# Kernel optimization log

Hardware: AMD Instinct MI355X
Metric: run time of the kernel (lower is better)

## Reference

```python
import jax, jax.numpy as jnp
import numpy as np

N = 100000   # nodes
E = 1600000  # edges
F = 13       # input features
H = 128      # hidden dim
G = 512      # graphs in batch
C = 10       # classes
EPS = 1e-5   # BatchNorm eps


def setup_inputs() -> dict:
    key = jax.random.key(0)
    ks = jax.random.split(key, 12)
    inp = {
        "x": jax.random.normal(ks[0], (N, F), dtype=jnp.float32),
        "edge_index": jax.random.randint(ks[1], (2, E), 0, N, dtype=jnp.int64),
        "batch": jnp.sort(jax.random.randint(ks[2], (N,), 0, G, dtype=jnp.int64)),
        "W1": jax.random.normal(ks[3], (F, H), dtype=jnp.float32) / np.sqrt(F),
        "b1": jnp.zeros((H,), jnp.float32),
        "g1": jnp.ones((H,), jnp.float32), "be1": jnp.zeros((H,), jnp.float32),
        "m1": jnp.zeros((H,), jnp.float32), "v1": jnp.ones((H,), jnp.float32),
        "W2": jax.random.normal(ks[4], (H, H), dtype=jnp.float32) / np.sqrt(H),
        "b2": jnp.zeros((H,), jnp.float32),
        "g2": jnp.ones((H,), jnp.float32), "be2": jnp.zeros((H,), jnp.float32),
        "m2": jnp.zeros((H,), jnp.float32), "v2": jnp.ones((H,), jnp.float32),
        "W3": jax.random.normal(ks[5], (H, H), dtype=jnp.float32) / np.sqrt(H),
        "b3": jnp.zeros((H,), jnp.float32),
        "g3": jnp.ones((H,), jnp.float32), "be3": jnp.zeros((H,), jnp.float32),
        "m3": jnp.zeros((H,), jnp.float32), "v3": jnp.ones((H,), jnp.float32),
        "Wc1": jax.random.normal(ks[6], (H, H // 2), dtype=jnp.float32) / np.sqrt(H),
        "bc1": jnp.zeros((H // 2,), jnp.float32),
        "Wc2": jax.random.normal(ks[7], (H // 2, C), dtype=jnp.float32) / np.sqrt(H // 2),
        "bc2": jnp.zeros((C,), jnp.float32),
    }
    return inp


def reference(x, edge_index, batch,
              W1, b1, g1, be1, m1, v1,
              W2, b2, g2, be2, m2, v2,
              W3, b3, g3, be3, m3, v3,
              Wc1, bc1, Wc2, bc2):
    src, dst = edge_index[0], edge_index[1]
    n = x.shape[0]
    # GCN symmetric norm with self-loops: deg = in-degree(A) + 1
    deg = jax.ops.segment_sum(jnp.ones(src.shape[0], x.dtype), dst, num_segments=n) + 1.0
    dis = jax.lax.rsqrt(deg)                    # D^{-1/2}
    enorm = dis[src] * dis[dst]                 # per-edge norm [E]
    snorm = dis * dis                           # self-loop norm [N]

    def gcn(h, W, b):
        h = h @ W                               # [N,H]
        msg = h[src] * enorm[:, None]           # gather + scale [E,H]
        agg = jax.ops.segment_sum(msg, dst, num_segments=n)  # scatter-add
        return agg + h * snorm[:, None] + b

    def bn(h, g, be, m, v):                     # eval-mode BatchNorm1d
        return (h - m) * jax.lax.rsqrt(v + EPS) * g + be

    h = jax.nn.relu(bn(gcn(x, W1, b1), g1, be1, m1, v1))
    h = jax.nn.relu(bn(gcn(h, W2, b2), g2, be2, m2, v2))
    h = jax.nn.relu(bn(gcn(h, W3, b3), g3, be3, m3, v3))
    # dropout is identity in eval mode

    # global mean pool over graphs
    sums = jax.ops.segment_sum(h, batch, num_segments=G)            # [G,H]
    cnts = jax.ops.segment_sum(jnp.ones(n, h.dtype), batch, num_segments=G)
    pooled = sums / jnp.maximum(cnts, 1.0)[:, None]

    hid = jax.nn.relu(pooled @ Wc1 + bc1)
    logits = hid @ Wc2 + bc2                                        # [G,C]
    return logits
```

## Files before the change

### kernel.cpp

```cpp
#include <hip/hip_runtime.h>
#include <hip/hip_bf16.h>

#define EPS 1e-5f

typedef unsigned short u16;
typedef unsigned int u32;
typedef __attribute__((ext_vector_type(8))) short bf16x8;
typedef __attribute__((ext_vector_type(4))) float f32x4;

__device__ __forceinline__ u32 f2bf(float f) {
  u32 u = __float_as_uint(f);
  return (u + 0x7FFFu + ((u >> 16) & 1u)) >> 16;
}
__device__ __forceinline__ u32 pack2bf(float lo, float hi) {
  return f2bf(lo) | (f2bf(hi) << 16);
}

__device__ __forceinline__ void dacc(float2& a, u32 u) {
  a.x += __uint_as_float(u << 16);
  a.y += __uint_as_float(u & 0xFFFF0000u);
}

__global__ void k_hist_rank(const int* __restrict__ dst, int* __restrict__ cnt,
                            int* __restrict__ rank, int E) {
  int i = blockIdx.x * blockDim.x + threadIdx.x;
  int i4 = i << 2;
  if (i4 + 3 < E) {
    int d0 = dst[i4], d1 = dst[i4 + 1], d2 = dst[i4 + 2], d3 = dst[i4 + 3];
    int r0 = atomicAdd(&cnt[d0], 1);
    int r1 = atomicAdd(&cnt[d1], 1);
    int r2 = atomicAdd(&cnt[d2], 1);
    int r3 = atomicAdd(&cnt[d3], 1);
    rank[i4] = r0; rank[i4 + 1] = r1; rank[i4 + 2] = r2; rank[i4 + 3] = r3;
  } else {
    for (int e = i4; e < E; ++e) rank[e] = atomicAdd(&cnt[dst[e]], 1);
  }
}

__global__ void k_dis_pdeg(const int* __restrict__ cnt, float* __restrict__ dis,
                           int* __restrict__ pdeg, int N) {
  int i = blockIdx.x * blockDim.x + threadIdx.x;
  if (i < N) {
    int d = cnt[i];
    dis[i] = rsqrtf((float)d + 1.0f);
    pdeg[i] = (d + 3) & ~3;
  }
}

__global__ void k_scan_block(const int* __restrict__ in, int* __restrict__ out,
                             int* __restrict__ bsum, int N) {
  __shared__ int tmp[256];
  int lid = threadIdx.x;
  int i = blockIdx.x * 256 + lid;
  int v = (i < N) ? in[i] : 0;
  tmp[lid] = v;
  __syncthreads();
  for (int off = 1; off < 256; off <<= 1) {
    int t = (lid >= off) ? tmp[lid - off] : 0;
    __syncthreads();
    tmp[lid] += t;
    __syncthreads();
  }
  if (i < N) out[i] = tmp[lid] - v;
  if (lid == 255) bsum[blockIdx.x] = tmp[255];
}

__global__ void k_scan_bsum(const int* __restrict__ bsum, int* __restrict__ bexc, int nb) {
  __shared__ int tmp[512];
  int lid = threadIdx.x;
  int v = (lid < nb) ? bsum[lid] : 0;
  tmp[lid] = v;
  __syncthreads();
  for (int off = 1; off < 512; off <<= 1) {
    int t = (lid >= off) ? tmp[lid - off] : 0;
    __syncthreads();
    tmp[lid] += t;
    __syncthreads();
  }
  if (lid < nb) bexc[lid] = tmp[lid] - v;
}

__global__ void k_add_back(int* __restrict__ offs, const int* __restrict__ bexc,
                           const int* __restrict__ bsum, int N, int nb) {
  int i = blockIdx.x * 256 + threadIdx.x;
  if (i < N) offs[i] += bexc[blockIdx.x];
  if (i == 0) offs[N] = bexc[nb - 1] + bsum[nb - 1];
}

__global__ void k_fill_rank(const int* __restrict__ src, const int* __restrict__ dst,
                            const int* __restrict__ rank, const int* __restrict__ offs,
                            int* __restrict__ csr, int E) {
  int i = blockIdx.x * blockDim.x + threadIdx.x;
  int i4 = i << 2;
  if (i4 + 3 < E) {
    int s0 = src[i4], s1 = src[i4 + 1], s2 = src[i4 + 2], s3 = src[i4 + 3];
    int d0 = dst[i4], d1 = dst[i4 + 1], d2 = dst[i4 + 2], d3 = dst[i4 + 3];
    int r0 = rank[i4], r1 = rank[i4 + 1], r2 = rank[i4 + 2], r3 = rank[i4 + 3];
    csr[offs[d0] + r0] = s0;
    csr[offs[d1] + r1] = s1;
    csr[offs[d2] + r2] = s2;
    csr[offs[d3] + r3] = s3;
  } else {
    for (int e = i4; e < E; ++e) csr[offs[dst[e]] + rank[e]] = src[e];
  }
}

__global__ void k_pad_fill(const int* __restrict__ deg, const int* __restrict__ offs,
                           int* __restrict__ csr, int N) {
  int n = blockIdx.x * blockDim.x + threadIdx.x;
  if (n >= N) return;
  int b = offs[n] + deg[n], e = offs[n + 1];
  for (int j = b; j < e; ++j) csr[j] = N;
}

__global__ void k_prep_w(const float* __restrict__ W2, const float* __restrict__ W3,
                         const float* __restrict__ b2, const float* __restrict__ g2,
                         const float* __restrict__ be2, const float* __restrict__ m2,
                         const float* __restrict__ v2,
                         const float* __restrict__ b3, const float* __restrict__ g3,
                         const float* __restrict__ be3, const float* __restrict__ m3,
                         const float* __restrict__ v3,
                         u16* __restrict__ Wht2, u16* __restrict__ Wlt2,
                         u16* __restrict__ Wht3, u16* __restrict__ Wlt3,
                         float* __restrict__ sc2, float* __restrict__ tc2,
                         float* __restrict__ sc3, float* __restrict__ tc3) {
  int idx = blockIdx.x * 256 + threadIdx.x;
  int layer = idx >> 14;
  int e = idx & 16383;
  int c = e >> 7, k = e & 127;
  const float* W = layer ? W3 : W2;
  float w = W[k * 128 + c];
  u32 h = f2bf(w);
  float l = w - __uint_as_float(h << 16);
  u16* Wh = layer ? Wht3 : Wht2;
  u16* Wl = layer ? Wlt3 : Wlt2;
  Wh[e] = (u16)h;
  Wl[e] = (u16)f2bf(l);
  if (e < 128) {
    int ch = e;
    const float* gg = layer ? g3 : g2;  const float* vv = layer ? v3 : v2;
    const float* be = layer ? be3 : be2; const float* mm = layer ? m3 : m2;
    const float* bb = layer ? b3 : b2;
    float s = gg[ch] * rsqrtf(vv[ch] + EPS);
    (layer ? sc3 : sc2)[ch] = s;
    (layer ? tc3 : tc2)[ch] = be[ch] + (bb[ch] - mm[ch]) * s;
  }
}

__global__ void k_padx_scale(const float* __restrict__ x, const float* __restrict__ dis,
                             float* __restrict__ xs, int N) {
  int i = blockIdx.x * blockDim.x + threadIdx.x;
  if (i >= (N + 1) * 16) return;
  int n = i >> 4, f = i & 15;
  xs[i] = (n < N && f < 13) ? x[n * 13 + f] * dis[n] : 0.0f;
}

__global__ __launch_bounds__(64) void k_agg16(
    const float* __restrict__ xs, const int* __restrict__ csr,
    const int* __restrict__ offs, const float* __restrict__ dis,
    float* __restrict__ out, int N) {
  int node = (blockIdx.x << 2) + (threadIdx.x >> 4);
  if (node >= N) return;
  int f = threadIdx.x & 15;
  float a0 = xs[(size_t)node * 16 + f];
  float a1 = 0.f, a2 = 0.f, a3 = 0.f;
  int beg = offs[node], end = offs[node + 1];
  for (int i = beg; i < end; i += 4) {
    int4 s4 = *(const int4*)(csr + i);
    a0 += xs[(size_t)s4.x * 16 + f];
    a1 += xs[(size_t)s4.y * 16 + f];
    a2 += xs[(size_t)s4.z * 16 + f];
    a3 += xs[(size_t)s4.w * 16 + f];
  }
  out[(size_t)node * 16 + f] = dis[node] * ((a0 + a1) + (a2 + a3));
}

__global__ __launch_bounds__(256) void k_gemm1(
    const float* __restrict__ ax, const float* __restrict__ W1,
    const float* __restrict__ bb, const float* __restrict__ gg,
    const float* __restrict__ be, const float* __restrict__ mm,
    const float* __restrict__ vv, const float* __restrict__ dis,
    u32* __restrict__ outb, int N) {
  const int lane = threadIdx.x & 63;
  const int wid = blockIdx.x * (blockDim.x >> 6) + (threadIdx.x >> 6);
  const int nw = gridDim.x * (blockDim.x >> 6);
  const int c0 = lane * 2, c1 = c0 + 1;
  float s0 = gg[c0] * rsqrtf(vv[c0] + EPS);
  float t0 = be[c0] + (bb[c0] - mm[c0]) * s0;
  float s1 = gg[c1] * rsqrtf(vv[c1] + EPS);
  float t1 = be[c1] + (bb[c1] - mm[c1]) * s1;
  float w0[13], w1[13];
#pragma unroll
  for (int k = 0; k < 13; ++k) {
    w0[k] = W1[k * 128 + c0];
    w1[k] = W1[k * 128 + c1];
  }
  for (int node = wid; node <= N; node += nw) {
    if (node == N) { outb[(size_t)node * 64 + lane] = 0u; continue; }
    float4 A0 = *(const float4*)(ax + (size_t)node * 16);
    float4 A1 = *(const float4*)(ax + (size_t)node * 16 + 4);
    float4 A2 = *(const float4*)(ax + (size_t)node * 16 + 8);
    float  a12 = ax[(size_t)node * 16 + 12];
    float av[13] = {A0.x, A0.y, A0.z, A0.w, A1.x, A1.y, A1.z, A1.w,
                    A2.x, A2.y, A2.z, A2.w, a12};
    float acc0 = 0.f, acc1 = 0.f;
#pragma unroll
    for (int k = 0; k < 13; ++k) {
      acc0 = fmaf(av[k], w0[k], acc0);
      acc1 = fmaf(av[k], w1[k], acc1);
    }
    float dn = dis[node];
    float o0 = dn * fmaxf(fmaf(acc0, s0, t0), 0.f);
    float o1 = dn * fmaxf(fmaf(acc1, s1, t1), 0.f);
    outb[(size_t)node * 64 + lane] = pack2bf(o0, o1);
  }
}

__global__ __launch_bounds__(256) void k_agg128(
    const u16* __restrict__ hb, const int* __restrict__ csr,
    const int* __restrict__ offs, const float* __restrict__ dis,
    uint4* __restrict__ Ahp, uint4* __restrict__ Alp, int N) {
  int node = (blockIdx.x << 2) + (threadIdx.x >> 6);
  if (node >= N) return;
  node = __builtin_amdgcn_readfirstlane(node);
  const int lane = threadIdx.x & 63;
  const int qt = lane >> 4;
  const int q = lane & 15;
  const uint4* __restrict__ H = (const uint4*)hb;
  int beg = offs[node], end = offs[node + 1];

  float2 z2 = make_float2(0.f, 0.f);
  float2 aA0 = z2, aA1 = z2, aA2 = z2, aA3 = z2;
  float2 aB0 = z2, aB1 = z2, aB2 = z2, aB3 = z2;

  {
    uint4 su = H[(size_t)node * 16 + q];
    if (qt == 0) { dacc(aA0, su.x); dacc(aA1, su.y); dacc(aA2, su.z); dacc(aA3, su.w); }
  }

  int i = beg;
  for (; i + 8 <= end; i += 8) {
    int4 sA = *(const int4*)(csr + i);
    int4 sB = *(const int4*)(csr + i + 4);
    int ea = (qt == 0) ? sA.x : (qt == 1) ? sA.y : (qt == 2) ? sA.z : sA.w;
    int eb = (qt == 0) ? sB.x : (qt == 1) ? sB.y : (qt == 2) ? sB.z : sB.w;
    uint4 uA = H[(size_t)ea * 16 + q];
    uint4 uB = H[(size_t)eb * 16 + q];
    dacc(aA0, uA.x); dacc(aA1, uA.y); dacc(aA2, uA.z); dacc(aA3, uA.w);
    dacc(aB0, uB.x); dacc(aB1, uB.y); dacc(aB2, uB.z); dacc(aB3, uB.w);
  }
  if (i < end) {
    int4 sA = *(const int4*)(csr + i);
    int ea = (qt == 0) ? sA.x : (qt == 1) ? sA.y : (qt == 2) ? sA.z : sA.w;
    uint4 uA = H[(size_t)ea * 16 + q];
    dacc(aA0, uA.x); dacc(aA1, uA.y); dacc(aA2, uA.z); dacc(aA3, uA.w);
  }

  float r[8];
  r[0] = aA0.x + aB0.x; r[1] = aA0.y + aB0.y;
  r[2] = aA1.x + aB1.x; r[3] = aA1.y + aB1.y;
  r[4] = aA2.x + aB2.x; r[5] = aA2.y + aB2.y;
  r[6] = aA3.x + aB3.x; r[7] = aA3.y + aB3.y;
#pragma unroll
  for (int j = 0; j < 8; ++j) {
    r[j] += __shfl_xor(r[j], 16, 64);
    r[j] += __shfl_xor(r[j], 32, 64);
  }
  if (qt == 0) {
    float dn = dis[node];
    uint4 ph, pl;
    u32 hw[8];
#pragma unroll
    for (int j = 0; j < 8; ++j) { r[j] *= dn; hw[j] = f2bf(r[j]); }
    ph.x = hw[0] | (hw[1] << 16);
    ph.y = hw[2] | (hw[3] << 16);
    ph.z = hw[4] | (hw[5] << 16);
    ph.w = hw[6] | (hw[7] << 16);
    float l[8];
#pragma unroll
    for (int j = 0; j < 8; ++j) l[j] = r[j] - __uint_as_float(hw[j] << 16);
    pl.x = pack2bf(l[0], l[1]);
    pl.y = pack2bf(l[2], l[3]);
    pl.z = pack2bf(l[4], l[5]);
    pl.w = pack2bf(l[6], l[7]);
    Ahp[(size_t)node * 16 + q] = ph;
    Alp[(size_t)node * 16 + q] = pl;
  }
}

template <bool OB>
__global__ __launch_bounds__(256) void k_gemm_mfma(
    const u16* __restrict__ Ah, const u16* __restrict__ Al,
    const u16* __restrict__ Wht, const u16* __restrict__ Wlt,
    const float* __restrict__ sc, const float* __restrict__ tc,
    const float* __restrict__ dis,
    float* __restrict__ outf, u16* __restrict__ outb, int N) {
  const int lane = threadIdx.x & 63;
  const int wv = threadIdx.x >> 6;
  const int r0 = blockIdx.x * 128 + wv * 32;
  const int lr = lane & 15;
  const int kg = lane >> 4;

  bf16x8 ahf[2][4], alf[2][4];
#pragma unroll
  for (int rt = 0; rt < 2; ++rt) {
    int row = min(r0 + rt * 16 + lr, N - 1);
    const bf16x8* pAh = (const bf16x8*)(Ah + (size_t)row * 128 + kg * 8);
    const bf16x8* pAl = (const bf16x8*)(Al + (size_t)row * 128 + kg * 8);
#pragma unroll
    for (int ks = 0; ks < 4; ++ks) {
      ahf[rt][ks] = pAh[ks * 4];
      alf[rt][ks] = pAl[ks * 4];
    }
  }
  float dr[2][4];
  if (OB) {
#pragma unroll
    for (int rt = 0; rt < 2; ++rt)
#pragma unroll
      for (int j = 0; j < 4; ++j)
        dr[rt][j] = dis[min(r0 + rt * 16 + kg * 4 + j, N - 1)];
  }

#pragma unroll
  for (int ct = 0; ct < 8; ++ct) {
    int c = ct * 16 + lr;
    const bf16x8* pBh = (const bf16x8*)(Wht + (size_t)c * 128 + kg * 8);
    const bf16x8* pBl = (const bf16x8*)(Wlt + (size_t)c * 128 + kg * 8);
    bf16x8 bh[4], bl[4];
#pragma unroll
    for (int ks = 0; ks < 4; ++ks) { bh[ks] = pBh[ks * 4]; bl[ks] = pBl[ks * 4]; }
    float s = sc[c], t = tc[c];
#pragma unroll
    for (int rt = 0; rt < 2; ++rt) {
      f32x4 acc = {0.f, 0.f, 0.f, 0.f};
#pragma unroll
      for (int ks = 0; ks < 4; ++ks) {
        acc = __builtin_amdgcn_mfma_f32_16x16x32_bf16(ahf[rt][ks], bh[ks], acc, 0, 0, 0);
        acc = __builtin_amdgcn_mfma_f32_16x16x32_bf16(alf[rt][ks], bh[ks], acc, 0, 0, 0);
        acc = __builtin_amdgcn_mfma_f32_16x16x32_bf16(ahf[rt][ks], bl[ks], acc, 0, 0, 0);
      }
#pragma unroll
      for (int j = 0; j < 4; ++j) {
        int row = r0 + rt * 16 + kg * 4 + j;
        if (row < N) {
          float o = fmaxf(fmaf(acc[j], s, t), 0.f);
          if (OB) {
            outb[(size_t)row * 128 + c] = (u16)f2bf(o * dr[rt][j]);
          } else {
            outf[(size_t)row * 128 + c] = o;
          }
        }
      }
    }
  }
}

__global__ void k_cnt_batch(const int* __restrict__ batch, int* __restrict__ cnt,
                            int N, int G) {
  int g = blockIdx.x * blockDim.x + threadIdx.x;
  if (g >= G) return;
  int lo = 0, hi = N;
  while (lo < hi) { int m = (lo + hi) >> 1; if (batch[m] < g) lo = m + 1; else hi = m; }
  int lb = lo;
  lo = 0; hi = N;
  while (lo < hi) { int m = (lo + hi) >> 1; if (batch[m] <= g) lo = m + 1; else hi = m; }
  cnt[g] = lo - lb;
}

__global__ __launch_bounds__(128) void k_pool(
    const float* __restrict__ h, const int* __restrict__ batch,
    float* __restrict__ pooled, int N) {
  int f = threadIdx.x;
  int n0 = blockIdx.x * 128;
  int nEnd = min(n0 + 128, N);
  float acc = 0.f;
  int cur = -1;
  for (int nn = n0; nn < nEnd; ++nn) {
    int g = batch[nn];
    if (g != cur) {
      if (cur >= 0) atomicAdd(&pooled[cur * 128 + f], acc);
      cur = g;
      acc = 0.f;
    }
    acc += h[(size_t)nn * 128 + f];
  }
  if (cur >= 0) atomicAdd(&pooled[cur * 128 + f], acc);
}

__global__ __launch_bounds__(64) void k_cls(
    const float* __restrict__ pooled, const int* __restrict__ cnt,
    const float* __restrict__ Wc1, const float* __restrict__ bc1,
    const float* __restrict__ Wc2, const float* __restrict__ bc2,
    float* __restrict__ out, int G) {
  __shared__ float pm[128];
  __shared__ float hid[64];
  int g = blockIdx.x, t = threadIdx.x;
  float invc = 1.f / fmaxf((float)cnt[g], 1.f);
  pm[t]      = pooled[g * 128 + t] * invc;
  pm[t + 64] = pooled[g * 128 + 64 + t] * invc;
  __syncthreads();
  float a = bc1[t];
#pragma unroll 8
  for (int k = 0; k < 128; ++k) a = fmaf(pm[k], Wc1[k * 64 + t], a);
  hid[t] = fmaxf(a, 0.f);
  __syncthreads();
  if (t < 10) {
    float a2 = bc2[t];
#pragma unroll
    for (int j = 0; j < 64; ++j) a2 = fmaf(hid[j], Wc2[j * 10 + t], a2);
    out[g * 10 + t] = a2;
  }
}

extern "C" void kernel_launch(void* const* d_in, const int* in_sizes, int n_in,
                              void* d_out, int out_size, void* d_ws, size_t ws_size,
                              hipStream_t stream) {
  const float* x   = (const float*)d_in[0];
  const int*   ei  = (const int*)d_in[1];
  const int* batch = (const int*)d_in[2];
  const float* W1 = (const float*)d_in[3];
  const float* b1 = (const float*)d_in[4];
  const float* g1 = (const float*)d_in[5];
  const float* be1 = (const float*)d_in[6];
  const float* m1 = (const float*)d_in[7];
  const float* v1 = (const float*)d_in[8];
  const float* W2 = (const float*)d_in[9];
  const float* b2 = (const float*)d_in[10];
  const float* g2 = (const float*)d_in[11];
  const float* be2 = (const float*)d_in[12];
  const float* m2 = (const float*)d_in[13];
  const float* v2 = (const float*)d_in[14];
  const float* W3 = (const float*)d_in[15];
  const float* b3 = (const float*)d_in[16];
  const float* g3 = (const float*)d_in[17];
  const float* be3 = (const float*)d_in[18];
  const float* m3 = (const float*)d_in[19];
  const float* v3 = (const float*)d_in[20];
  const float* Wc1 = (const float*)d_in[21];
  const float* bc1 = (const float*)d_in[22];
  const float* Wc2 = (const float*)d_in[23];
  const float* bc2 = (const float*)d_in[24];

  const int N = in_sizes[0] / 13;
  const int E = in_sizes[1] / 2;
  const int G = out_size / 10;
  const int* src = ei;
  const int* dst = ei + E;

  char* ws = (char*)d_ws;
  size_t off = 0;
  auto alloc = [&](size_t bytes) {
    char* p = ws + off;
    off = (off + bytes + 255) & ~(size_t)255;
    return p;
  };
  int*   deg    = (int*)  alloc((size_t)N * 4);
  float* dis    = (float*)alloc((size_t)N * 4);
  int*   pdeg   = (int*)  alloc((size_t)N * 4);
  int*   offs   = (int*)  alloc((size_t)(N + 1) * 4);
  const int nb  = (N + 255) / 256;
  int*   bsum   = (int*)  alloc((size_t)nb * 4);
  int*   bexc   = (int*)  alloc((size_t)nb * 4);
  int*   rank   = (int*)  alloc((size_t)E * 4);
  int*   csr    = (int*)  alloc(((size_t)E + 3 * (size_t)N + 8) * 4);
  u16*   hbf    = (u16*)  alloc((size_t)(N + 1) * 128 * 2);
  u16*   Ahp    = (u16*)  alloc((size_t)N * 128 * 2);
  u16*   Alp    = (u16*)  alloc((size_t)N * 128 * 2);
  float* bufF   = (float*)alloc((size_t)(N + 1) * 128 * 4);
  u16*   Wht2   = (u16*)  alloc(16384 * 2);
  u16*   Wlt2   = (u16*)  alloc(16384 * 2);
  u16*   Wht3   = (u16*)  alloc(16384 * 2);
  u16*   Wlt3   = (u16*)  alloc(16384 * 2);
  float* sc2    = (float*)alloc(128 * 4);
  float* tc2    = (float*)alloc(128 * 4);
  float* sc3    = (float*)alloc(128 * 4);
  float* tc3    = (float*)alloc(128 * 4);
  float* pooled = (float*)alloc((size_t)G * 128 * 4);
  int*   cntg   = (int*)  alloc((size_t)G * 4);
  float* xs = bufF;
  float* ax = (float*)Ahp;

  hipMemsetAsync(deg, 0, (size_t)N * 4, stream);
  hipMemsetAsync(pooled, 0, (size_t)G * 128 * 4, stream);

  k_prep_w<<<128, 256, 0, stream>>>(W2, W3, b2, g2, be2, m2, v2, b3, g3, be3, m3, v3,
                                    Wht2, Wlt2, Wht3, Wlt3, sc2, tc2, sc3, tc3);

  const int nE4 = (E + 3) / 4;
  k_hist_rank<<<(nE4 + 255) / 256, 256, 0, stream>>>(dst, deg, rank, E);
  k_dis_pdeg<<<(N + 255) / 256, 256, 0, stream>>>(deg, dis, pdeg, N);
  k_scan_block<<<nb, 256, 0, stream>>>(pdeg, offs, bsum, N);
  k_scan_bsum<<<1, 512, 0, stream>>>(bsum, bexc, nb);
  k_add_back<<<nb, 256, 0, stream>>>(offs, bexc, bsum, N, nb);
  k_fill_rank<<<(nE4 + 255) / 256, 256, 0, stream>>>(src, dst, rank, offs, csr, E);
  k_pad_fill<<<(N + 255) / 256, 256, 0, stream>>>(deg, offs, csr, N);

  k_padx_scale<<<((N + 1) * 16 + 255) / 256, 256, 0, stream>>>(x, dis, xs, N);
  k_agg16<<<(N + 3) / 4, 64, 0, stream>>>(xs, csr, offs, dis, ax, N);
  k_gemm1<<<1024, 256, 0, stream>>>(ax, W1, b1, g1, be1, m1, v1, dis, (u32*)hbf, N);

  const int gemmGrid = (N + 127) / 128;
  k_agg128<<<(N + 3) / 4, 256, 0, stream>>>(hbf, csr, offs, dis,
                                            (uint4*)Ahp, (uint4*)Alp, N);
  k_gemm_mfma<true><<<gemmGrid, 256, 0, stream>>>(Ahp, Alp, Wht2, Wlt2, sc2, tc2, dis,
                                                  nullptr, hbf, N);
  k_agg128<<<(N + 3) / 4, 256, 0, stream>>>(hbf, csr, offs, dis,
                                            (uint4*)Ahp, (uint4*)Alp, N);
  k_gemm_mfma<false><<<gemmGrid, 256, 0, stream>>>(Ahp, Alp, Wht3, Wlt3, sc3, tc3, dis,
                                                   bufF, nullptr, N);

  k_cnt_batch<<<(G + 255) / 256, 256, 0, stream>>>(batch, cntg, N, G);
  k_pool<<<(N + 127) / 128, 128, 0, stream>>>(bufF, batch, pooled, N);
  k_cls<<<G, 64, 0, stream>>>(pooled, cntg, Wc1, bc1, Wc2, bc2, (float*)d_out, G);
}
```

Measured before the change: 540.3 us.

## Fuse preprocessing kernels and store final layer output as bf16

Merges the degree-norm and x-scaling kernels into one per-node kernel, folds CSR padding fill into the scan add-back, and moves graph count binary search into the classifier kernel, which removes several launches. The histogram kernel now handles 8 edges per thread with vector loads and stores. The last GCN layer writes bf16 instead of fp32, so pooling reads half the bytes, at the cost of extra rounding error in the pooled features.

```diff
diff --git a/kernel.cpp b/kernel.cpp
--- a/kernel.cpp
+++ b/kernel.cpp
@@ -24,27 +24,47 @@
 __global__ void k_hist_rank(const int* __restrict__ dst, int* __restrict__ cnt,
                             int* __restrict__ rank, int E) {
   int i = blockIdx.x * blockDim.x + threadIdx.x;
-  int i4 = i << 2;
-  if (i4 + 3 < E) {
-    int d0 = dst[i4], d1 = dst[i4 + 1], d2 = dst[i4 + 2], d3 = dst[i4 + 3];
-    int r0 = atomicAdd(&cnt[d0], 1);
-    int r1 = atomicAdd(&cnt[d1], 1);
-    int r2 = atomicAdd(&cnt[d2], 1);
-    int r3 = atomicAdd(&cnt[d3], 1);
-    rank[i4] = r0; rank[i4 + 1] = r1; rank[i4 + 2] = r2; rank[i4 + 3] = r3;
+  int i8 = i << 3;
+  if (i8 + 7 < E) {
+    int4 da = *(const int4*)(dst + i8);
+    int4 db = *(const int4*)(dst + i8 + 4);
+    int r0 = atomicAdd(&cnt[da.x], 1);
+    int r1 = atomicAdd(&cnt[da.y], 1);
+    int r2 = atomicAdd(&cnt[da.z], 1);
+    int r3 = atomicAdd(&cnt[da.w], 1);
+    int r4 = atomicAdd(&cnt[db.x], 1);
+    int r5 = atomicAdd(&cnt[db.y], 1);
+    int r6 = atomicAdd(&cnt[db.z], 1);
+    int r7 = atomicAdd(&cnt[db.w], 1);
+    *(int4*)(rank + i8)     = make_int4(r0, r1, r2, r3);
+    *(int4*)(rank + i8 + 4) = make_int4(r4, r5, r6, r7);
   } else {
-    for (int e = i4; e < E; ++e) rank[e] = atomicAdd(&cnt[dst[e]], 1);
-  }
-}
-
-__global__ void k_dis_pdeg(const int* __restrict__ cnt, float* __restrict__ dis,
-                           int* __restrict__ pdeg, int N) {
-  int i = blockIdx.x * blockDim.x + threadIdx.x;
-  if (i < N) {
-    int d = cnt[i];
-    dis[i] = rsqrtf((float)d + 1.0f);
-    pdeg[i] = (d + 3) & ~3;
-  }
+    for (int e = i8; e < E; ++e) rank[e] = atomicAdd(&cnt[dst[e]], 1);
+  }
+}
+
+__global__ void k_prep_nodes(const int* __restrict__ cnt, const float* __restrict__ x,
+                             float* __restrict__ dis, int* __restrict__ pdeg,
+                             float* __restrict__ xs, int N) {
+  int n = blockIdx.x * blockDim.x + threadIdx.x;
+  if (n > N) return;
+  if (n == N) {
+#pragma unroll
+    for (int f = 0; f < 16; f += 4)
+      *(float4*)(xs + (size_t)N * 16 + f) = make_float4(0.f, 0.f, 0.f, 0.f);
+    return;
+  }
+  int d = cnt[n];
+  float dn = rsqrtf((float)d + 1.0f);
+  dis[n] = dn;
+  pdeg[n] = (d + 3) & ~3;
+  float v[16];
+#pragma unroll
+  for (int f = 0; f < 13; ++f) v[f] = x[(size_t)n * 13 + f] * dn;
+  v[13] = v[14] = v[15] = 0.f;
+#pragma unroll
+  for (int f = 0; f < 16; f += 4)
+    *(float4*)(xs + (size_t)n * 16 + f) = make_float4(v[f], v[f+1], v[f+2], v[f+3]);
 }
 
 __global__ void k_scan_block(const int* __restrict__ in, int* __restrict__ out,
@@ -80,10 +100,17 @@
   if (lid < nb) bexc[lid] = tmp[lid] - v;
 }
 
-__global__ void k_add_back(int* __restrict__ offs, const int* __restrict__ bexc,
-                           const int* __restrict__ bsum, int N, int nb) {
+__global__ void k_add_back_pad(int* __restrict__ offs, const int* __restrict__ bexc,
+                               const int* __restrict__ bsum, const int* __restrict__ deg,
+                               const int* __restrict__ pdeg, int* __restrict__ csr,
+                               int N, int nb) {
   int i = blockIdx.x * 256 + threadIdx.x;
-  if (i < N) offs[i] += bexc[blockIdx.x];
+  if (i < N) {
+    int o = offs[i] + bexc[blockIdx.x];
+    offs[i] = o;
+    int b = o + deg[i], e = o + pdeg[i];
+    for (int j = b; j < e; ++j) csr[j] = N;
+  }
   if (i == 0) offs[N] = bexc[nb - 1] + bsum[nb - 1];
 }
 
@@ -103,14 +130,6 @@
   } else {
     for (int e = i4; e < E; ++e) csr[offs[dst[e]] + rank[e]] = src[e];
   }
-}
-
-__global__ void k_pad_fill(const int* __restrict__ deg, const int* __restrict__ offs,
-                           int* __restrict__ csr, int N) {
-  int n = blockIdx.x * blockDim.x + threadIdx.x;
-  if (n >= N) return;
-  int b = offs[n] + deg[n], e = offs[n + 1];
-  for (int j = b; j < e; ++j) csr[j] = N;
 }
 
 __global__ void k_prep_w(const float* __restrict__ W2, const float* __restrict__ W3,
@@ -147,14 +166,6 @@
   }
 }
 
-__global__ void k_padx_scale(const float* __restrict__ x, const float* __restrict__ dis,
-                             float* __restrict__ xs, int N) {
-  int i = blockIdx.x * blockDim.x + threadIdx.x;
-  if (i >= (N + 1) * 16) return;
-  int n = i >> 4, f = i & 15;
-  xs[i] = (n < N && f < 13) ? x[n * 13 + f] * dis[n] : 0.0f;
-}
-
 __global__ __launch_bounds__(64) void k_agg16(
     const float* __restrict__ xs, const int* __restrict__ csr,
     const int* __restrict__ offs, const float* __restrict__ dis,
@@ -288,13 +299,13 @@
   }
 }
 
-template <bool OB>
+template <int MODE>
 __global__ __launch_bounds__(256) void k_gemm_mfma(
     const u16* __restrict__ Ah, const u16* __restrict__ Al,
     const u16* __restrict__ Wht, const u16* __restrict__ Wlt,
     const float* __restrict__ sc, const float* __restrict__ tc,
     const float* __restrict__ dis,
-    float* __restrict__ outf, u16* __restrict__ outb, int N) {
+    u16* __restrict__ outb, int N) {
   const int lane = threadIdx.x & 63;
   const int wv = threadIdx.x >> 6;
   const int r0 = blockIdx.x * 128 + wv * 32;
@@ -314,7 +325,7 @@
     }
   }
   float dr[2][4];
-  if (OB) {
+  if (MODE == 0) {
 #pragma unroll
     for (int rt = 0; rt < 2; ++rt)
 #pragma unroll
@@ -345,31 +356,16 @@
         int row = r0 + rt * 16 + kg * 4 + j;
         if (row < N) {
           float o = fmaxf(fmaf(acc[j], s, t), 0.f);
-          if (OB) {
-            outb[(size_t)row * 128 + c] = (u16)f2bf(o * dr[rt][j]);
-          } else {
-            outf[(size_t)row * 128 + c] = o;
-          }
+          if (MODE == 0) o *= dr[rt][j];
+          outb[(size_t)row * 128 + c] = (u16)f2bf(o);
         }
       }
     }
   }
 }
 
-__global__ void k_cnt_batch(const int* __restrict__ batch, int* __restrict__ cnt,
-                            int N, int G) {
-  int g = blockIdx.x * blockDim.x + threadIdx.x;
-  if (g >= G) return;
-  int lo = 0, hi = N;
-  while (lo < hi) { int m = (lo + hi) >> 1; if (batch[m] < g) lo = m + 1; else hi = m; }
-  int lb = lo;
-  lo = 0; hi = N;
-  while (lo < hi) { int m = (lo + hi) >> 1; if (batch[m] <= g) lo = m + 1; else hi = m; }
-  cnt[g] = lo - lb;
-}
-
 __global__ __launch_bounds__(128) void k_pool(
-    const float* __restrict__ h, const int* __restrict__ batch,
+    const u16* __restrict__ hb, const int* __restrict__ batch,
     float* __restrict__ pooled, int N) {
   int f = threadIdx.x;
   int n0 = blockIdx.x * 128;
@@ -383,20 +379,30 @@
       cur = g;
       acc = 0.f;
     }
-    acc += h[(size_t)nn * 128 + f];
+    acc += __uint_as_float((u32)hb[(size_t)nn * 128 + f] << 16);
   }
   if (cur >= 0) atomicAdd(&pooled[cur * 128 + f], acc);
 }
 
 __global__ __launch_bounds__(64) void k_cls(
-    const float* __restrict__ pooled, const int* __restrict__ cnt,
+    const float* __restrict__ pooled, const int* __restrict__ batch, int N,
     const float* __restrict__ Wc1, const float* __restrict__ bc1,
     const float* __restrict__ Wc2, const float* __restrict__ bc2,
     float* __restrict__ out, int G) {
   __shared__ float pm[128];
   __shared__ float hid[64];
+  __shared__ float invc_s;
   int g = blockIdx.x, t = threadIdx.x;
-  float invc = 1.f / fmaxf((float)cnt[g], 1.f);
+  if (t == 0) {
+    int lo = 0, hi = N;
+    while (lo < hi) { int m = (lo + hi) >> 1; if (batch[m] < g) lo = m + 1; else hi = m; }
+    int lb = lo;
+    lo = 0; hi = N;
+    while (lo < hi) { int m = (lo + hi) >> 1; if (batch[m] <= g) lo = m + 1; else hi = m; }
+    invc_s = 1.f / fmaxf((float)(lo - lb), 1.f);
+  }
+  __syncthreads();
+  float invc = invc_s;
   pm[t]      = pooled[g * 128 + t] * invc;
   pm[t + 64] = pooled[g * 128 + 64 + t] * invc;
   __syncthreads();
@@ -467,7 +473,7 @@
   u16*   hbf    = (u16*)  alloc((size_t)(N + 1) * 128 * 2);
   u16*   Ahp    = (u16*)  alloc((size_t)N * 128 * 2);
   u16*   Alp    = (u16*)  alloc((size_t)N * 128 * 2);
-  float* bufF   = (float*)alloc((size_t)(N + 1) * 128 * 4);
+  float* xs     = (float*)alloc((size_t)(N + 1) * 16 * 4);
   u16*   Wht2   = (u16*)  alloc(16384 * 2);
   u16*   Wlt2   = (u16*)  alloc(16384 * 2);
   u16*   Wht3   = (u16*)  alloc(16384 * 2);
@@ -477,8 +483,6 @@
   float* sc3    = (float*)alloc(128 * 4);
   float* tc3    = (float*)alloc(128 * 4);
   float* pooled = (float*)alloc((size_t)G * 128 * 4);
-  int*   cntg   = (int*)  alloc((size_t)G * 4);
-  float* xs = bufF;
   float* ax = (float*)Ahp;
 
   hipMemsetAsync(deg, 0, (size_t)N * 4, stream);
@@ -487,30 +491,28 @@
   k_prep_w<<<128, 256, 0, stream>>>(W2, W3, b2, g2, be2, m2, v2, b3, g3, be3, m3, v3,
                                     Wht2, Wlt2, Wht3, Wlt3, sc2, tc2, sc3, tc3);
 
-  const int nE4 = (E + 3) / 4;
-  k_hist_rank<<<(nE4 + 255) / 256, 256, 0, stream>>>(dst, deg, rank, E);
-  k_dis_pdeg<<<(N + 255) / 256, 256, 0, stream>>>(deg, dis, pdeg, N);
+  const int nE8 = (E + 7) / 8;
+  k_hist_rank<<<(nE8 + 255) / 256, 256, 0, stream>>>(dst, deg, rank, E);
+  k_prep_nodes<<<(N + 256) / 256, 256, 0, stream>>>(deg, x, dis, pdeg, xs, N);
   k_scan_block<<<nb, 256, 0, stream>>>(pdeg, offs, bsum, N);
   k_scan_bsum<<<1, 512, 0, stream>>>(bsum, bexc, nb);
-  k_add_back<<<nb, 256, 0, stream>>>(offs, bexc, bsum, N, nb);
+  k_add_back_pad<<<nb, 256, 0, stream>>>(offs, bexc, bsum, deg, pdeg, csr, N, nb);
+  const int nE4 = (E + 3) / 4;
   k_fill_rank<<<(nE4 + 255) / 256, 256, 0, stream>>>(src, dst, rank, offs, csr, E);
-  k_pad_fill<<<(N + 255) / 256, 256, 0, stream>>>(deg, offs, csr, N);
-
-  k_padx_scale<<<((N + 1) * 16 + 255) / 256, 256, 0, stream>>>(x, dis, xs, N);
+
   k_agg16<<<(N + 3) / 4, 64, 0, stream>>>(xs, csr, offs, dis, ax, N);
   k_gemm1<<<1024, 256, 0, stream>>>(ax, W1, b1, g1, be1, m1, v1, dis, (u32*)hbf, N);
 
   const int gemmGrid = (N + 127) / 128;
   k_agg128<<<(N + 3) / 4, 256, 0, stream>>>(hbf, csr, offs, dis,
                                             (uint4*)Ahp, (uint4*)Alp, N);
-  k_gemm_mfma<true><<<gemmGrid, 256, 0, stream>>>(Ahp, Alp, Wht2, Wlt2, sc2, tc2, dis,
-                                                  nullptr, hbf, N);
+  k_gemm_mfma<0><<<gemmGrid, 256, 0, stream>>>(Ahp, Alp, Wht2, Wlt2, sc2, tc2, dis,
+                                               hbf, N);
   k_agg128<<<(N + 3) / 4, 256, 0, stream>>>(hbf, csr, offs, dis,
                                             (uint4*)Ahp, (uint4*)Alp, N);
-  k_gemm_mfma<false><<<gemmGrid, 256, 0, stream>>>(Ahp, Alp, Wht3, Wlt3, sc3, tc3, dis,
-                                                   bufF, nullptr, N);
-
-  k_cnt_batch<<<(G + 255) / 256, 256, 0, stream>>>(batch, cntg, N, G);
-  k_pool<<<(N + 127) / 128, 128, 0, stream>>>(bufF, batch, pooled, N);
-  k_cls<<<G, 64, 0, stream>>>(pooled, cntg, Wc1, bc1, Wc2, bc2, (float*)d_out, G);
-}
+  k_gemm_mfma<1><<<gemmGrid, 256, 0, stream>>>(Ahp, Alp, Wht3, Wlt3, sc3, tc3, dis,
+                                               hbf, N);
+
+  k_pool<<<(N + 127) / 128, 128, 0, stream>>>(hbf, batch, pooled, N);
+  k_cls<<<G, 64, 0, stream>>>(pooled, batch, N, Wc1, bc1, Wc2, bc2, (float*)d_out, G);
+}
```

New measurement: 532.6 us. No clear change (-1.4%).
